# Kernel optimization log

Measured on AMD Instinct MI355X. Metric: run time of the kernel, lower is better.

The kernel has to match this reference:

```python
import jax, jax.numpy as jnp
import numpy as np

NUM_ENT = 50000
NUM_REL = 200          # init_rel has 2*NUM_REL rows (fwd + inverse)
D = 200                # init_dim = gcn_dim = embed_dim
B = 1024
E_HALF = 250000        # edges per direction; total 2*E_HALF
PERM = 1
K_H, K_W = 20, 10      # 2*k_w*k_h == 2*embed_dim
NUM_FILT = 96
KER = 9
FLAT_SZ = K_H * 2 * K_W * NUM_FILT * PERM  # 38400


def _bn(x, g, b, axes):
    # batch-norm with batch statistics (training-mode math, no running stats)
    m = jnp.mean(x, axes, keepdims=True)
    v = jnp.var(x, axes, keepdims=True)
    return (x - m) * jax.lax.rsqrt(v + 1e-5) * g + b


def setup_inputs() -> dict:
    key = jax.random.key(0)
    ks = jax.random.split(key, 24)
    rng = np.random.default_rng(0)
    # graph (constants)
    s = jax.random.randint(ks[0], (E_HALF,), 0, NUM_ENT)
    d = jax.random.randint(ks[1], (E_HALF,), 0, NUM_ENT)
    t = jax.random.randint(ks[2], (E_HALF,), 0, NUM_REL)
    edge_index = jnp.stack([jnp.concatenate([s, d]), jnp.concatenate([d, s])])  # [2, 2*E_HALF]
    edge_type = jnp.concatenate([t, t + NUM_REL])
    chequer_perm = jnp.asarray(np.stack([rng.permutation(2 * D) for _ in range(PERM)]), dtype=jnp.int32)
    # batch indices
    sub = jax.random.randint(ks[3], (B,), 0, NUM_ENT)
    rel = jax.random.randint(ks[4], (B,), 0, 2 * NUM_REL)
    neg_ents = jax.random.randint(ks[5], (B,), 0, NUM_ENT)
    n = lambda k, shp, sc=0.05: jax.random.normal(ks[k], shp, jnp.float32) * sc
    return {
        'sub': sub, 'rel': rel, 'neg_ents': neg_ents,
        'edge_index': edge_index, 'edge_type': edge_type, 'chequer_perm': chequer_perm,
        'init_embed': n(6, (NUM_ENT, D)),
        'init_rel': n(7, (2 * NUM_REL, D)),
        'w_in': n(8, (D, D)), 'w_out': n(9, (D, D)), 'w_loop': n(10, (D, D)),
        'w_rel': n(11, (D, D)), 'loop_rel': n(12, (1, D)),
        'bn0_g': jnp.ones((PERM,)), 'bn0_b': jnp.zeros((PERM,)),
        'bn1_g': jnp.ones((NUM_FILT * PERM,)), 'bn1_b': jnp.zeros((NUM_FILT * PERM,)),
        'bn2_g': jnp.ones((D,)), 'bn2_b': jnp.zeros((D,)),
        'conv_filt': n(13, (NUM_FILT, 1, KER, KER), 0.1),
        'fc_w': n(14, (D, FLAT_SZ), 0.01), 'fc_b': jnp.zeros((D,)),
        'bias_ent': jnp.zeros((NUM_ENT,)),
    }


def _forward(init_embed, init_rel, w_in, w_out, w_loop, w_rel, loop_rel,
             bn0_g, bn0_b, bn1_g, bn1_b, bn2_g, bn2_b,
             conv_filt, fc_w, fc_b, bias_ent,
             sub, rel, edge_index, edge_type, chequer_perm):
    # ---- GPKGConv encoder (CompGCN-style, op='sub', eval mode -> dropout off) ----
    src, dst = edge_index[0], edge_index[1]
    msg = init_embed[src] - init_rel[edge_type]                      # [E, D] irregular gather
    msg = jnp.concatenate([msg[:E_HALF] @ w_in, msg[E_HALF:] @ w_out], axis=0)
    deg = jax.ops.segment_sum(jnp.ones(msg.shape[0], msg.dtype), dst, num_segments=NUM_ENT)
    dinv = jnp.where(deg > 0, jax.lax.rsqrt(jnp.maximum(deg, 1.0)), 0.0)
    norm = (dinv[src] * dinv[dst])[:, None]
    agg = jax.ops.segment_sum(msg * norm, dst, num_segments=NUM_ENT)  # irregular scatter
    loop_msg = (init_embed - loop_rel) @ w_loop
    all_ent = jnp.tanh((agg + loop_msg) / 3.0)                        # [num_ent, D]
    r = init_rel @ w_rel                                              # [2*num_rel, D]
    # ---- InteractE-style chequer conv decoder ----
    sub_emb = all_ent[sub]
    rel_emb = r[rel]
    comb = jnp.concatenate([sub_emb, rel_emb], axis=1)                # [B, 2D]
    cheq = jnp.take(comb, chequer_perm, axis=1)                       # [B, perm, 2D]
    x = cheq.reshape(-1, PERM, 2 * K_W, K_H)
    x = _bn(x, bn0_g.reshape(1, -1, 1, 1), bn0_b.reshape(1, -1, 1, 1), (0, 2, 3))
    pad = KER // 2
    x = jnp.pad(x, ((0, 0), (0, 0), (pad, pad), (pad, pad)), mode='wrap')  # circular pad
    filt = jnp.tile(conv_filt, (PERM, 1, 1, 1))
    x = jax.lax.conv_general_dilated(x, filt, (1, 1), 'VALID',
                                     dimension_numbers=('NCHW', 'OIHW', 'NCHW'),
                                     feature_group_count=PERM)        # [B, 96, 20, 20]
    x = _bn(x, bn1_g.reshape(1, -1, 1, 1), bn1_b.reshape(1, -1, 1, 1), (0, 2, 3))
    x = jax.nn.relu(x)
    x = x.reshape(x.shape[0], -1) @ fc_w.T + fc_b                     # [B, D]
    x = _bn(x, bn2_g, bn2_b, (0,))
    x = jax.nn.relu(x)
    logits = x @ all_ent.T + bias_ent                                 # [B, num_ent]
    return jax.nn.sigmoid(logits)


def reference(sub, rel, neg_ents, edge_index, edge_type, chequer_perm,
              init_embed, init_rel, w_in, w_out, w_loop, w_rel, loop_rel,
              bn0_g, bn0_b, bn1_g, bn1_b, bn2_g, bn2_b,
              conv_filt, fc_w, fc_b, bias_ent):
    return _forward(init_embed, init_rel, w_in, w_out, w_loop, w_rel, loop_rel,
                    bn0_g, bn0_b, bn1_g, bn1_b, bn2_g, bn2_b,
                    conv_filt, fc_w, fc_b, bias_ent,
                    sub, rel, edge_index, edge_type, chequer_perm)
```

## Files before the change

### kernel.cpp

```cpp
#include <hip/hip_runtime.h>

#define ETOT  500000
#define EHALF 250000
#define NENT  50000
#define NSEG  (2 * NENT)
#define DD    200
#define BB    1024
#define NF    96
#define FLAT  38400

#define FC_KS     20
#define FC_KSLICE 1920
#define FC_NCHUNK 60

#define LE 64

#define OFF_AGG      0LL
#define ZSTART       20000000LL
#define OFF_CNT      20000000LL
#define OFF_ACC0     20100004LL
#define OFF_ACC1     20100006LL
#define ZEND         20100198LL
#define OFF_CURSOR   20304998LL
#define OFF_BSUM     20404998LL
#define OFF_ELIST    20405126LL
#define OFF_WT       20405128LL
#define OFF_DINV     20905126LL
#define OFF_RMAT     20955126LL
#define OFF_CHEQ     21035126LL
#define OFF_BN1S     21444726LL
#define OFF_X2H      21649720LL
#define OFF_X2L      21752120LL

#define OD_CONV 0LL
#define OD_FWH  39321600LL
#define OD_FWL  43161600LL
#define OD_PART 47001600LL

typedef __attribute__((ext_vector_type(8))) short bf16x8;
typedef __attribute__((ext_vector_type(4))) float f32x4;

__device__ inline void bf16split(float v, ushort& h, ushort& l) {
    unsigned u = __float_as_uint(v);
    unsigned hu = u & 0xffff0000u;
    h = (ushort)(hu >> 16);
    float lf = v - __uint_as_float(hu);
    l = (ushort)(__float_as_uint(lf) >> 16);
}

__device__ inline void split8(const float* e, bf16x8& h8, bf16x8& l8) {
#pragma unroll
    for (int t = 0; t < 8; t++) {
        ushort h, l;
        bf16split(e[t], h, l);
        h8[t] = (short)h;
        l8[t] = (short)l;
    }
}


__global__ void k_hist(const int* __restrict__ ei, int* __restrict__ cnt) {
    int e = blockIdx.x * 256 + threadIdx.x;
    if (e < ETOT) {
        int seg = (e < EHALF ? 0 : NENT) + ei[ETOT + e];
        atomicAdd(&cnt[seg], 1);
    }
}

__global__ void k_dinv(const int* __restrict__ cnt, float* __restrict__ dinv) {
    int i = blockIdx.x * 256 + threadIdx.x;
    if (i < NENT) {
        int d = cnt[i] + cnt[NENT + i];
        dinv[i] = d > 0 ? rsqrtf((float)d) : 0.f;
    }
}

__global__ void k_scan1(int* __restrict__ cnt, int* __restrict__ bsum) {
    __shared__ int S[256];
    int base = blockIdx.x * 1024 + threadIdx.x * 4;
    int v[4], s = 0;
#pragma unroll
    for (int i = 0; i < 4; i++) { v[i] = (base + i <= NSEG) ? cnt[base + i] : 0; s += v[i]; }
    S[threadIdx.x] = s;
    __syncthreads();
    for (int off = 1; off < 256; off <<= 1) {
        int t = (threadIdx.x >= off) ? S[threadIdx.x - off] : 0;
        __syncthreads();
        S[threadIdx.x] += t;
        __syncthreads();
    }
    int run = S[threadIdx.x] - s;
#pragma unroll
    for (int i = 0; i < 4; i++) {
        if (base + i <= NSEG) cnt[base + i] = run;
        run += v[i];
    }
    if (threadIdx.x == 255) bsum[blockIdx.x] = S[255];
}

__global__ void k_scan2(int* __restrict__ bsum) {
    __shared__ int S[128];
    int v = (threadIdx.x < 98) ? bsum[threadIdx.x] : 0;
    S[threadIdx.x] = v;
    __syncthreads();
    for (int off = 1; off < 128; off <<= 1) {
        int t = (threadIdx.x >= off) ? S[threadIdx.x - off] : 0;
        __syncthreads();
        S[threadIdx.x] += t;
        __syncthreads();
    }
    if (threadIdx.x < 98) bsum[threadIdx.x] = S[threadIdx.x] - v;
}

__global__ void k_scan3(int* __restrict__ cnt, const int* __restrict__ bsum,
                        int* __restrict__ cursor) {
    int add = bsum[blockIdx.x];
    int base = blockIdx.x * 1024 + threadIdx.x * 4;
#pragma unroll
    for (int i = 0; i < 4; i++) {
        int idx = base + i;
        if (idx <= NSEG) {
            int v = cnt[idx] + add;
            cnt[idx] = v;
            if (idx < NSEG) cursor[idx] = v;
        }
    }
}

__global__ void k_fill(const int* __restrict__ ei, int* __restrict__ cursor,
                       int* __restrict__ elist) {
    int e = blockIdx.x * 256 + threadIdx.x;
    if (e < ETOT) {
        int seg = (e < EHALF ? 0 : NENT) + ei[ETOT + e];
        int pos = atomicAdd(&cursor[seg], 1);
        elist[pos] = e;
    }
}

__global__ void k_agg(const int* __restrict__ ei, const int* __restrict__ et,
                      const int* __restrict__ row_start, const int* __restrict__ elist,
                      const float* __restrict__ emb, const float* __restrict__ rel,
                      const float* __restrict__ dinv, float* __restrict__ agg) {
    int seg = blockIdx.x * 4 + (threadIdx.x >> 6);
    int lane = threadIdx.x & 63;
    int dst = seg - (seg >= NENT ? NENT : 0);
    float dd = dinv[dst];
    int s = row_start[seg], e = row_start[seg + 1];
    bool act = lane < 50;
    float4 acc = {0.f, 0.f, 0.f, 0.f};
    for (int i = s; i < e; i++) {
        int ed = elist[i];
        int src = ei[ed];
        int t = et[ed];
        float nrm = dinv[src] * dd;
        if (act) {
            float4 a = *(const float4*)&emb[(long long)src * DD + lane * 4];
            float4 b = *(const float4*)&rel[t * DD + lane * 4];
            acc.x += (a.x - b.x) * nrm;
            acc.y += (a.y - b.y) * nrm;
            acc.z += (a.z - b.z) * nrm;
            acc.w += (a.w - b.w) * nrm;
        }
    }
    if (act) *(float4*)&agg[(long long)seg * DD + lane * 4] = acc;
}


__global__ void k_cvt3w(const float* __restrict__ w_in, const float* __restrict__ w_out,
                        const float* __restrict__ w_loop,
                        ushort* __restrict__ wth, ushort* __restrict__ wtl) {
    int idx = blockIdx.x * 256 + threadIdx.x;
    if (idx >= 3 * DD * DD) return;
    int s = idx / (DD * DD);
    int rem = idx - s * DD * DD;
    int j = rem / DD, k = rem - (rem / DD) * DD;
    const float* w = (s == 0) ? w_in : (s == 1) ? w_out : w_loop;
    ushort h, l;
    bf16split(w[k * DD + j], h, l);
    wth[idx] = h;
    wtl[idx] = l;
}

__global__ __launch_bounds__(256) void k_allent_mfma(
        const float* __restrict__ agg, const float* __restrict__ emb,
        const float* __restrict__ loop_rel,
        const ushort* __restrict__ wth, const ushort* __restrict__ wtl,
        float* __restrict__ all_ent) {
    __shared__ __align__(16) ushort Bh[2][112][36];
    __shared__ __align__(16) ushort Bl[2][112][36];
    __shared__ float lr[DD];
    int tid = threadIdx.x;
    for (int i = tid; i < DD; i += 256) lr[i] = loop_rel[i];
    int wid = tid >> 6, lane = tid & 63, l15 = lane & 15, q = lane >> 4;
    int r0 = blockIdx.x * 64;
    int nh = blockIdx.y;
    int row = r0 + wid * 16 + l15;
    if (row > NENT - 1) row = NENT - 1;
    const float* apa = &agg[(long long)row * DD];
    const float* apb = &agg[(long long)(NENT + row) * DD];
    const float* apc = &emb[(long long)row * DD];

    bool stg = tid < 224;
    int srow = tid - (tid >= 112 ? 112 : 0);
    if (srow > 111) srow = 0;
    bool spl = (tid >= 112) && stg;
    int sj = nh * 112 + srow;
    int sjr = sj < DD ? sj : DD - 1;
    const ushort* bplane = spl ? wtl : wth;
    int srowoff = sjr * DD;
    ushort* d0 = spl ? &Bl[0][srow][0] : &Bh[0][srow][0];
    ushort* d1 = spl ? &Bl[1][srow][0] : &Bh[1][srow][0];

    f32x4 zero4 = {0.f, 0.f, 0.f, 0.f};
    f32x4 acc[7];
#pragma unroll
    for (int n = 0; n < 7; n++) acc[n] = zero4;

    uint4 w0 = {0u,0u,0u,0u}, w1 = {0u,0u,0u,0u}, w2 = {0u,0u,0u,0u}, w3 = {0u,0u,0u,0u};
    if (stg) {
        const ushort* src = bplane + srowoff;
        w0 = *(const uint4*)&src[0];
        w1 = *(const uint4*)&src[8];
        w2 = *(const uint4*)&src[16];
        w3 = *(const uint4*)&src[24];
        *(uint4*)&d0[0]  = w0;
        *(uint4*)&d0[8]  = w1;
        *(uint4*)&d0[16] = w2;
        *(uint4*)&d0[24] = w3;
    }
    float4 a1, a2;
    {
        int k0 = q * 8;
        a1 = *(const float4*)&apa[k0];
        a2 = *(const float4*)&apa[k0 + 4];
    }
    __syncthreads();

    for (int t = 0; t < 21; t++) {
        int buf = t & 1;
        int s = t / 7, kk = t - s * 7;
        bool prt = (kk == 6);
        int k0 = prt ? 192 : kk * 32 + q * 8;
        bool act = !prt || (q == 0);
        bool more = (t + 1 < 21);
        if (stg && more) {
            int t2 = t + 1, ss = t2 / 7, k2 = t2 - ss * 7;
            bool p2 = (k2 == 6);
            int koff2 = p2 ? 192 : k2 * 32;
            const ushort* src = bplane + ss * (DD * DD) + srowoff + koff2;
            uint4 zz = {0u,0u,0u,0u};
            w0 = *(const uint4*)&src[0];
            w1 = p2 ? zz : *(const uint4*)&src[8];
            w2 = p2 ? zz : *(const uint4*)&src[16];
            w3 = p2 ? zz : *(const uint4*)&src[24];
        }
        float4 n1 = {0.f, 0.f, 0.f, 0.f}, n2 = {0.f, 0.f, 0.f, 0.f};
        if (more) {
            int t2 = t + 1, ss = t2 / 7, k2 = t2 - ss * 7;
            bool p2 = (k2 == 6);
            int ka = p2 ? 192 : k2 * 32 + q * 8;
            const float* apn = (ss == 0) ? apa : (ss == 1) ? apb : apc;
            if (!p2 || q == 0) {
                n1 = *(const float4*)&apn[ka];
                n2 = *(const float4*)&apn[ka + 4];
            }
        }
        float e[8] = {0.f, 0.f, 0.f, 0.f, 0.f, 0.f, 0.f, 0.f};
        if (act) {
            float4 v1 = a1, v2 = a2;
            if (s == 2) {
                float4 u1 = *(const float4*)&lr[k0];
                float4 u2 = *(const float4*)&lr[k0 + 4];
                v1.x -= u1.x; v1.y -= u1.y; v1.z -= u1.z; v1.w -= u1.w;
                v2.x -= u2.x; v2.y -= u2.y; v2.z -= u2.z; v2.w -= u2.w;
            }
            e[0] = v1.x; e[1] = v1.y; e[2] = v1.z; e[3] = v1.w;
            e[4] = v2.x; e[5] = v2.y; e[6] = v2.z; e[7] = v2.w;
        }
        bf16x8 ah, al;
        split8(e, ah, al);
#pragma unroll
        for (int n = 0; n < 7; n++) {
            bf16x8 bh = *(const bf16x8*)&Bh[buf][n * 16 + l15][q * 8];
            bf16x8 bl = *(const bf16x8*)&Bl[buf][n * 16 + l15][q * 8];
            acc[n] = __builtin_amdgcn_mfma_f32_16x16x32_bf16(ah, bh, acc[n], 0, 0, 0);
            acc[n] = __builtin_amdgcn_mfma_f32_16x16x32_bf16(ah, bl, acc[n], 0, 0, 0);
            acc[n] = __builtin_amdgcn_mfma_f32_16x16x32_bf16(al, bh, acc[n], 0, 0, 0);
        }
        if (stg && more) {
            ushort* d = buf ? d0 : d1;
            *(uint4*)&d[0]  = w0;
            *(uint4*)&d[8]  = w1;
            *(uint4*)&d[16] = w2;
            *(uint4*)&d[24] = w3;
        }
        __syncthreads();
        a1 = n1; a2 = n2;
    }
#pragma unroll
    for (int n = 0; n < 7; n++) {
        int j = nh * 112 + n * 16 + l15;
        if (j < DD) {
            int rowb = r0 + wid * 16 + q * 4;
#pragma unroll
            for (int r = 0; r < 4; r++) {
                if (rowb + r < NENT)
                    all_ent[(long long)(rowb + r) * DD + j] = tanhf(acc[n][r] * (1.f / 3.f));
            }
        }
    }
}

__global__ void k_cvt(const float* __restrict__ src, ushort* __restrict__ hi,
                      ushort* __restrict__ lo) {
    long long i = (long long)(blockIdx.x * 256 + threadIdx.x) * 4;
    if (i >= (long long)NENT * DD) return;
    float4 v = *(const float4*)&src[i];
    ushort4 h, l;
    bf16split(v.x, h.x, l.x);
    bf16split(v.y, h.y, l.y);
    bf16split(v.z, h.z, l.z);
    bf16split(v.w, h.w, l.w);
    *(ushort4*)&hi[i] = h;
    *(ushort4*)&lo[i] = l;
}

__global__ void k_cvtw(const float* __restrict__ src, ushort* __restrict__ hi,
                       ushort* __restrict__ lo) {
    long long i = (long long)(blockIdx.x * 256 + threadIdx.x) * 4;
    if (i >= (long long)DD * FLAT) return;
    float4 v = *(const float4*)&src[i];
    ushort4 h, l;
    bf16split(v.x, h.x, l.x);
    bf16split(v.y, h.y, l.y);
    bf16split(v.z, h.z, l.z);
    bf16split(v.w, h.w, l.w);
    *(ushort4*)&hi[i] = h;
    *(ushort4*)&lo[i] = l;
}

__global__ void k_rmat(const float* __restrict__ init_rel, const float* __restrict__ w_rel,
                       float* __restrict__ rmat) {
    __shared__ float S[16][DD];
    int r0 = blockIdx.x * 16;
    for (int i = threadIdx.x; i < 16 * DD; i += 256)
        S[i / DD][i % DD] = init_rel[(r0 + i / DD) * DD + i % DD];
    __syncthreads();
    int j = threadIdx.x;
    if (j < DD) {
        float acc[16];
#pragma unroll
        for (int rr = 0; rr < 16; rr++) acc[rr] = 0.f;
        for (int k = 0; k < DD; k += 4) {
            float wx = w_rel[(k + 0) * DD + j], wy = w_rel[(k + 1) * DD + j],
                  wz = w_rel[(k + 2) * DD + j], ww = w_rel[(k + 3) * DD + j];
#pragma unroll
            for (int rr = 0; rr < 16; rr++) {
                float4 a = *(const float4*)&S[rr][k];
                acc[rr] += a.x * wx + a.y * wy + a.z * wz + a.w * ww;
            }
        }
#pragma unroll
        for (int rr = 0; rr < 16; rr++) rmat[(r0 + rr) * DD + j] = acc[rr];
    }
}


__global__ void k_cheq(const int* __restrict__ sub, const int* __restrict__ rel,
                       const int* __restrict__ perm, const float* __restrict__ all_ent,
                       const float* __restrict__ rmat, float* __restrict__ cheq,
                       float* __restrict__ acc0) {
    int i = blockIdx.x * 256 + threadIdx.x;
    int b = i / 400, p = i % 400;
    int c = perm[p];
    float v = (c < DD) ? all_ent[(long long)sub[b] * DD + c]
                       : rmat[rel[b] * DD + (c - DD)];
    cheq[i] = v;
    __shared__ float s1[256], s2[256];
    s1[threadIdx.x] = v;
    s2[threadIdx.x] = v * v;
    __syncthreads();
    for (int st = 128; st > 0; st >>= 1) {
        if (threadIdx.x < st) { s1[threadIdx.x] += s1[threadIdx.x + st]; s2[threadIdx.x] += s2[threadIdx.x + st]; }
        __syncthreads();
    }
    if (threadIdx.x == 0) { atomicAdd(&acc0[0], s1[0]); atomicAdd(&acc0[1], s2[0]); }
}

__global__ void k_conv(const float* __restrict__ cheq, const float* __restrict__ acc0,
                       const float* __restrict__ bn0_g, const float* __restrict__ bn0_b,
                       const float* __restrict__ filt, float* __restrict__ conv_out,
                       float* __restrict__ acc1) {
    __shared__ __align__(16) float xp[28][36];
    __shared__ float fl[NF * 81];
    __shared__ float csum[NF], csq[NF];
    int b = blockIdx.x;
    const float invN = 1.f / (BB * 400.f);
    float mean = acc0[0] * invN;
    float var = acc0[1] * invN - mean * mean;
    float sc = rsqrtf(var + 1e-5f) * bn0_g[0];
    float sh = bn0_b[0] - mean * sc;
    for (int i = threadIdx.x; i < 28 * 28; i += 256) {
        int r = i / 28, c = i % 28;
        int rr = (r + 16) % 20, cc = (c + 16) % 20;
        xp[r][c] = cheq[b * 400 + rr * 20 + cc] * sc + sh;
    }
    for (int i = threadIdx.x; i < NF * 81; i += 256) fl[i] = filt[i];
    if (threadIdx.x < NF) { csum[threadIdx.x] = 0.f; csq[threadIdx.x] = 0.f; }
    __syncthreads();
    for (int t = threadIdx.x; t < NF * 20; t += 256) {
        int ch = t / 20, row = t % 20;
        float acc[20];
#pragma unroll
        for (int c2 = 0; c2 < 20; c2++) acc[c2] = 0.f;
        for (int di = 0; di < 9; di++) {
            float xr[28];
#pragma unroll
            for (int g = 0; g < 7; g++) {
                float4 v = *(const float4*)&xp[row + di][g * 4];
                xr[g * 4 + 0] = v.x; xr[g * 4 + 1] = v.y;
                xr[g * 4 + 2] = v.z; xr[g * 4 + 3] = v.w;
            }
            float f[9];
#pragma unroll
            for (int dj = 0; dj < 9; dj++) f[dj] = fl[ch * 81 + di * 9 + dj];
#pragma unroll
            for (int dj = 0; dj < 9; dj++)
#pragma unroll
                for (int c2 = 0; c2 < 20; c2++)
                    acc[c2] = fmaf(xr[c2 + dj], f[dj], acc[c2]);
        }
        float s = 0.f, q = 0.f;
        long long base = (long long)b * FLAT + ch * 400 + row * 20;
#pragma unroll
        for (int c2 = 0; c2 < 20; c2++) {
            float v = acc[c2];
            s += v; q += v * v;
            conv_out[base + c2] = v;
        }
        atomicAdd(&csum[ch], s);
        atomicAdd(&csq[ch], q);
    }
    __syncthreads();
    if (threadIdx.x < NF) {
        atomicAdd(&acc1[threadIdx.x], csum[threadIdx.x]);
        atomicAdd(&acc1[NF + threadIdx.x], csq[threadIdx.x]);
    }
}

__global__ void k_bn1fin(const float* __restrict__ acc1, const float* __restrict__ g1,
                         const float* __restrict__ b1, float* __restrict__ bn1s) {
    int c = threadIdx.x;
    if (c >= NF) return;
    const float invN = 1.f / (BB * 400.f);
    float m = acc1[c] * invN;
    float v = acc1[NF + c] * invN - m * m;
    float sc = rsqrtf(v + 1e-5f) * g1[c];
    bn1s[c] = sc;
    bn1s[NF + c] = b1[c] - m * sc;
}

__global__ __launch_bounds__(256) void k_fc_mfma(
        const float* __restrict__ conv_out, const float* __restrict__ bn1s,
        const ushort* __restrict__ fwh, const ushort* __restrict__ fwl,
        float* __restrict__ part) {
    __shared__ __align__(16) ushort Bh[2][112][36];
    __shared__ __align__(16) ushort Bl[2][112][36];
    __shared__ float bns[192];
    int tid = threadIdx.x;
    for (int i = tid; i < 192; i += 256) bns[i] = bn1s[i];
    int wid = tid >> 6, lane = tid & 63, l15 = lane & 15, q = lane >> 4;
    int b0 = blockIdx.x * 64;
    int nh = blockIdx.y;
    int ksl = blockIdx.z;
    int kbase = ksl * FC_KSLICE;

    const float* ap = conv_out + (long long)(b0 + wid * 16 + l15) * FLAT;

    bool stg = tid < 224;
    int srow = tid - (tid >= 112 ? 112 : 0);
    if (srow > 111) srow = 0;
    bool spl = (tid >= 112) && stg;
    int sj = nh * 112 + srow;
    int sjr = sj < DD ? sj : DD - 1;
    const ushort* bsrc = (spl ? fwl : fwh) + (long long)sjr * FLAT + kbase;
    ushort* d0 = spl ? &Bl[0][srow][0] : &Bh[0][srow][0];
    ushort* d1 = spl ? &Bl[1][srow][0] : &Bh[1][srow][0];

    f32x4 zero4 = {0.f, 0.f, 0.f, 0.f};
    f32x4 acc[7];
#pragma unroll
    for (int n = 0; n < 7; n++) acc[n] = zero4;

    uint4 s0 = {0u,0u,0u,0u}, s1 = {0u,0u,0u,0u}, s2 = {0u,0u,0u,0u}, s3 = {0u,0u,0u,0u};
    if (stg) {
        s0 = *(const uint4*)&bsrc[0];
        s1 = *(const uint4*)&bsrc[8];
        s2 = *(const uint4*)&bsrc[16];
        s3 = *(const uint4*)&bsrc[24];
        *(uint4*)&d0[0]  = s0;
        *(uint4*)&d0[8]  = s1;
        *(uint4*)&d0[16] = s2;
        *(uint4*)&d0[24] = s3;
    }
    float4 a1, a2;
    {
        int k0 = kbase + q * 8;
        a1 = *(const float4*)&ap[k0];
        a2 = *(const float4*)&ap[k0 + 4];
    }
    __syncthreads();

    for (int c = 0; c < FC_NCHUNK; c++) {
        int buf = c & 1;
        int kc = kbase + c * 32 + q * 8;
        bool more = (c + 1 < FC_NCHUNK);
        if (stg && more) {
            int kn = (c + 1) * 32;
            s0 = *(const uint4*)&bsrc[kn];
            s1 = *(const uint4*)&bsrc[kn + 8];
            s2 = *(const uint4*)&bsrc[kn + 16];
            s3 = *(const uint4*)&bsrc[kn + 24];
        }
        float4 n1 = {0.f, 0.f, 0.f, 0.f}, n2 = {0.f, 0.f, 0.f, 0.f};
        if (more) {
            n1 = *(const float4*)&ap[kc + 32];
            n2 = *(const float4*)&ap[kc + 36];
        }
        int ch = kc / 400;
        float sc = bns[ch], sh = bns[96 + ch];
        float e[8] = {
            fmaxf(a1.x * sc + sh, 0.f), fmaxf(a1.y * sc + sh, 0.f),
            fmaxf(a1.z * sc + sh, 0.f), fmaxf(a1.w * sc + sh, 0.f),
            fmaxf(a2.x * sc + sh, 0.f), fmaxf(a2.y * sc + sh, 0.f),
            fmaxf(a2.z * sc + sh, 0.f), fmaxf(a2.w * sc + sh, 0.f)};
        bf16x8 ah, al;
        split8(e, ah, al);
#pragma unroll
        for (int n = 0; n < 7; n++) {
            bf16x8 bh = *(const bf16x8*)&Bh[buf][n * 16 + l15][q * 8];
            bf16x8 bl = *(const bf16x8*)&Bl[buf][n * 16 + l15][q * 8];
            acc[n] = __builtin_amdgcn_mfma_f32_16x16x32_bf16(ah, bh, acc[n], 0, 0, 0);
            acc[n] = __builtin_amdgcn_mfma_f32_16x16x32_bf16(ah, bl, acc[n], 0, 0, 0);
            acc[n] = __builtin_amdgcn_mfma_f32_16x16x32_bf16(al, bh, acc[n], 0, 0, 0);
        }
        if (stg && more) {
            ushort* d = buf ? d0 : d1;
            *(uint4*)&d[0]  = s0;
            *(uint4*)&d[8]  = s1;
            *(uint4*)&d[16] = s2;
            *(uint4*)&d[24] = s3;
        }
        __syncthreads();
        a1 = n1; a2 = n2;
    }
    long long pbase = (long long)ksl * (BB * DD);
#pragma unroll
    for (int n = 0; n < 7; n++) {
        int j = nh * 112 + n * 16 + l15;
        if (j < DD) {
            int rowb = b0 + wid * 16 + q * 4;
#pragma unroll
            for (int r = 0; r < 4; r++)
                part[pbase + (long long)(rowb + r) * DD + j] = acc[n][r];
        }
    }
}

__global__ void k_bn2(const float* __restrict__ part, const float* __restrict__ fc_b,
                      const float* __restrict__ g2, const float* __restrict__ b2,
                      ushort* __restrict__ x2h, ushort* __restrict__ x2l) {
    int j = blockIdx.x;
    float vals[4];
    float s = 0.f, q = 0.f;
#pragma unroll
    for (int i = 0; i < 4; i++) {
        int b = threadIdx.x + i * 256;
        float v = fc_b[j];
#pragma unroll
        for (int ks = 0; ks < FC_KS; ks++)
            v += part[(long long)ks * (BB * DD) + (long long)b * DD + j];
        vals[i] = v;
        s += v; q += v * v;
    }
    __shared__ float r1[256], r2[256];
    __shared__ float bc[2];
    r1[threadIdx.x] = s; r2[threadIdx.x] = q;
    __syncthreads();
    for (int st = 128; st > 0; st >>= 1) {
        if (threadIdx.x < st) { r1[threadIdx.x] += r1[threadIdx.x + st]; r2[threadIdx.x] += r2[threadIdx.x + st]; }
        __syncthreads();
    }
    if (threadIdx.x == 0) {
        float m = r1[0] * (1.f / BB);
        float v = r2[0] * (1.f / BB) - m * m;
        float sc = rsqrtf(v + 1e-5f) * g2[j];
        bc[0] = sc; bc[1] = b2[j] - m * sc;
    }
    __syncthreads();
    float sc = bc[0], sh = bc[1];
#pragma unroll
    for (int i = 0; i < 4; i++) {
        int b = threadIdx.x + i * 256;
        float v = fmaxf(vals[i] * sc + sh, 0.f);
        ushort h, l;
        bf16split(v, h, l);
        x2h[b * DD + j] = h;
        x2l[b * DD + j] = l;
    }
}

__global__ __launch_bounds__(512) void k_logits_mfma(
        const ushort* __restrict__ x2h, const ushort* __restrict__ x2l,
        const ushort* __restrict__ aeh, const ushort* __restrict__ ael,
        const float* __restrict__ bias, float* __restrict__ out) {
    __shared__ ushort Bhs[LE * DD];
    __shared__ ushort Bls[LE * DD];
    __shared__ __align__(16) float Tw[8][16][36];
    int e0 = blockIdx.x * LE;
    for (int i = threadIdx.x; i < 2 * LE * 25; i += 512) {
        int pl = i >= LE * 25;
        int ii = pl ? i - LE * 25 : i;
        int row = ii / 25, seg = ii % 25;
        int e = e0 + row;
        if (e > NENT - 1) e = NENT - 1;
        const ushort* src = (pl ? ael : aeh) + (long long)e * DD + seg * 8;
        uint4 v = *(const uint4*)src;
        if (pl) *(uint4*)&Bls[row * DD + seg * 8] = v;
        else    *(uint4*)&Bhs[row * DD + seg * 8] = v;
    }
    __syncthreads();

    int wid = threadIdx.x >> 6;
    int lane = threadIdx.x & 63;
    int l15 = lane & 15, q = lane >> 4;
    int wm = wid >> 1;
    int wn = wid & 1;

    int nbase0 = (wn * 32 + l15) * DD;
    int nbase1 = (wn * 32 + 16 + l15) * DD;

    int tr = lane >> 3;
    int tc = (lane & 7) * 4;
    int ceg = e0 + wn * 32 + tc;
    bool cval = ceg < NENT;
    float4 bb = {0.f, 0.f, 0.f, 0.f};
    if (cval) bb = *(const float4*)&bias[ceg];

    f32x4 zero4 = {0.f, 0.f, 0.f, 0.f};
    bf16x8 zf = {0, 0, 0, 0, 0, 0, 0, 0};
    const int STEP = 128 * DD;

    const ushort* ah0 = x2h + (long long)(wm * 32 + l15) * DD;
    const ushort* al0 = x2l + (long long)(wm * 32 + l15) * DD;
    const ushort* ah1 = ah0 + 16 * DD;
    const ushort* al1 = al0 + 16 * DD;

    bf16x8 pa_h0, pa_l0, pa_h1, pa_l1;
    {
        int k0 = q * 8;
        pa_h0 = *(const bf16x8*)&ah0[k0];
        pa_l0 = *(const bf16x8*)&al0[k0];
        pa_h1 = *(const bf16x8*)&ah1[k0];
        pa_l1 = *(const bf16x8*)&al1[k0];
    }

    for (int it = 0; it < 8; it++) {
        f32x4 acc00 = zero4, acc01 = zero4, acc10 = zero4, acc11 = zero4;
#pragma unroll
        for (int kk = 0; kk < 6; kk++) {
            int kn = (kk < 5) ? (kk + 1) * 32 + q * 8 : 192;
            bf16x8 na_h0 = *(const bf16x8*)&ah0[kn];
            bf16x8 na_l0 = *(const bf16x8*)&al0[kn];
            bf16x8 na_h1 = *(const bf16x8*)&ah1[kn];
            bf16x8 na_l1 = *(const bf16x8*)&al1[kn];
            int kb = kk * 32 + q * 8;
            bf16x8 bh0 = *(const bf16x8*)&Bhs[nbase0 + kb];
            bf16x8 bl0 = *(const bf16x8*)&Bls[nbase0 + kb];
            bf16x8 bh1 = *(const bf16x8*)&Bhs[nbase1 + kb];
            bf16x8 bl1 = *(const bf16x8*)&Bls[nbase1 + kb];
            acc00 = __builtin_amdgcn_mfma_f32_16x16x32_bf16(pa_h0, bh0, acc00, 0, 0, 0);
            acc00 = __builtin_amdgcn_mfma_f32_16x16x32_bf16(pa_h0, bl0, acc00, 0, 0, 0);
            acc00 = __builtin_amdgcn_mfma_f32_16x16x32_bf16(pa_l0, bh0, acc00, 0, 0, 0);
            acc01 = __builtin_amdgcn_mfma_f32_16x16x32_bf16(pa_h0, bh1, acc01, 0, 0, 0);
            acc01 = __builtin_amdgcn_mfma_f32_16x16x32_bf16(pa_h0, bl1, acc01, 0, 0, 0);
            acc01 = __builtin_amdgcn_mfma_f32_16x16x32_bf16(pa_l0, bh1, acc01, 0, 0, 0);
            acc10 = __builtin_amdgcn_mfma_f32_16x16x32_bf16(pa_h1, bh0, acc10, 0, 0, 0);
            acc10 = __builtin_amdgcn_mfma_f32_16x16x32_bf16(pa_h1, bl0, acc10, 0, 0, 0);
            acc10 = __builtin_amdgcn_mfma_f32_16x16x32_bf16(pa_l1, bh0, acc10, 0, 0, 0);
            acc11 = __builtin_amdgcn_mfma_f32_16x16x32_bf16(pa_h1, bh1, acc11, 0, 0, 0);
            acc11 = __builtin_amdgcn_mfma_f32_16x16x32_bf16(pa_h1, bl1, acc11, 0, 0, 0);
            acc11 = __builtin_amdgcn_mfma_f32_16x16x32_bf16(pa_l1, bh1, acc11, 0, 0, 0);
            pa_h0 = na_h0; pa_l0 = na_l0; pa_h1 = na_h1; pa_l1 = na_l1;
        }
        {
            bf16x8 na_h0 = zf, na_l0 = zf, na_h1 = zf, na_l1 = zf;
            if (it + 1 < 8) {
                int k0 = q * 8;
                na_h0 = *(const bf16x8*)&ah0[STEP + k0];
                na_l0 = *(const bf16x8*)&al0[STEP + k0];
                na_h1 = *(const bf16x8*)&ah1[STEP + k0];
                na_l1 = *(const bf16x8*)&al1[STEP + k0];
            }
            bool a0 = (q == 0);
            bf16x8 xh0 = a0 ? pa_h0 : zf, xl0 = a0 ? pa_l0 : zf;
            bf16x8 xh1 = a0 ? pa_h1 : zf, xl1 = a0 ? pa_l1 : zf;
            bf16x8 bh0 = a0 ? *(const bf16x8*)&Bhs[nbase0 + 192] : zf;
            bf16x8 bl0 = a0 ? *(const bf16x8*)&Bls[nbase0 + 192] : zf;
            bf16x8 bh1 = a0 ? *(const bf16x8*)&Bhs[nbase1 + 192] : zf;
            bf16x8 bl1 = a0 ? *(const bf16x8*)&Bls[nbase1 + 192] : zf;
            acc00 = __builtin_amdgcn_mfma_f32_16x16x32_bf16(xh0, bh0, acc00, 0, 0, 0);
            acc00 = __builtin_amdgcn_mfma_f32_16x16x32_bf16(xh0, bl0, acc00, 0, 0, 0);
            acc00 = __builtin_amdgcn_mfma_f32_16x16x32_bf16(xl0, bh0, acc00, 0, 0, 0);
            acc01 = __builtin_amdgcn_mfma_f32_16x16x32_bf16(xh0, bh1, acc01, 0, 0, 0);
            acc01 = __builtin_amdgcn_mfma_f32_16x16x32_bf16(xh0, bl1, acc01, 0, 0, 0);
            acc01 = __builtin_amdgcn_mfma_f32_16x16x32_bf16(xl0, bh1, acc01, 0, 0, 0);
            acc10 = __builtin_amdgcn_mfma_f32_16x16x32_bf16(xh1, bh0, acc10, 0, 0, 0);
            acc10 = __builtin_amdgcn_mfma_f32_16x16x32_bf16(xh1, bl0, acc10, 0, 0, 0);
            acc10 = __builtin_amdgcn_mfma_f32_16x16x32_bf16(xl1, bh0, acc10, 0, 0, 0);
            acc11 = __builtin_amdgcn_mfma_f32_16x16x32_bf16(xh1, bh1, acc11, 0, 0, 0);
            acc11 = __builtin_amdgcn_mfma_f32_16x16x32_bf16(xh1, bl1, acc11, 0, 0, 0);
            acc11 = __builtin_amdgcn_mfma_f32_16x16x32_bf16(xl1, bh1, acc11, 0, 0, 0);
            pa_h0 = na_h0; pa_l0 = na_l0; pa_h1 = na_h1; pa_l1 = na_l1;
        }
        {
#pragma unroll
            for (int r = 0; r < 4; r++) {
                Tw[wid][q * 4 + r][l15] = acc00[r];
                Tw[wid][q * 4 + r][16 + l15] = acc01[r];
            }
            float4 v0 = *(const float4*)&Tw[wid][tr][tc];
            float4 v1 = *(const float4*)&Tw[wid][8 + tr][tc];
            if (cval) {
                int rg0 = it * 128 + wm * 32 + tr;
                float4 o0, o1;
                o0.x = 1.f / (1.f + __expf(-(v0.x + bb.x)));
                o0.y = 1.f / (1.f + __expf(-(v0.y + bb.y)));
                o0.z = 1.f / (1.f + __expf(-(v0.z + bb.z)));
                o0.w = 1.f / (1.f + __expf(-(v0.w + bb.w)));
                o1.x = 1.f / (1.f + __expf(-(v1.x + bb.x)));
                o1.y = 1.f / (1.f + __expf(-(v1.y + bb.y)));
                o1.z = 1.f / (1.f + __expf(-(v1.z + bb.z)));
                o1.w = 1.f / (1.f + __expf(-(v1.w + bb.w)));
                *(float4*)&out[(long long)rg0 * NENT + ceg] = o0;
                *(float4*)&out[(long long)(rg0 + 8) * NENT + ceg] = o1;
            }
        }
        {
#pragma unroll
            for (int r = 0; r < 4; r++) {
                Tw[wid][q * 4 + r][l15] = acc10[r];
                Tw[wid][q * 4 + r][16 + l15] = acc11[r];
            }
            float4 v0 = *(const float4*)&Tw[wid][tr][tc];
            float4 v1 = *(const float4*)&Tw[wid][8 + tr][tc];
            if (cval) {
                int rg0 = it * 128 + wm * 32 + 16 + tr;
                float4 o0, o1;
                o0.x = 1.f / (1.f + __expf(-(v0.x + bb.x)));
                o0.y = 1.f / (1.f + __expf(-(v0.y + bb.y)));
                o0.z = 1.f / (1.f + __expf(-(v0.z + bb.z)));
                o0.w = 1.f / (1.f + __expf(-(v0.w + bb.w)));
                o1.x = 1.f / (1.f + __expf(-(v1.x + bb.x)));
                o1.y = 1.f / (1.f + __expf(-(v1.y + bb.y)));
                o1.z = 1.f / (1.f + __expf(-(v1.z + bb.z)));
                o1.w = 1.f / (1.f + __expf(-(v1.w + bb.w)));
                *(float4*)&out[(long long)rg0 * NENT + ceg] = o0;
                *(float4*)&out[(long long)(rg0 + 8) * NENT + ceg] = o1;
            }
        }
        ah0 += STEP; al0 += STEP; ah1 += STEP; al1 += STEP;
    }
}


extern "C" void kernel_launch(void* const* d_in, const int* in_sizes, int n_in,
                              void* d_out, int out_size, void* d_ws, size_t ws_size,
                              hipStream_t stream) {
    const int*   sub      = (const int*)d_in[0];
    const int*   rel      = (const int*)d_in[1];
    const int*   ei       = (const int*)d_in[3];
    const int*   et       = (const int*)d_in[4];
    const int*   perm     = (const int*)d_in[5];
    const float* emb      = (const float*)d_in[6];
    const float* init_rel = (const float*)d_in[7];
    const float* w_in     = (const float*)d_in[8];
    const float* w_out    = (const float*)d_in[9];
    const float* w_loop   = (const float*)d_in[10];
    const float* w_rel    = (const float*)d_in[11];
    const float* loop_rel = (const float*)d_in[12];
    const float* bn0_g    = (const float*)d_in[13];
    const float* bn0_b    = (const float*)d_in[14];
    const float* bn1_g    = (const float*)d_in[15];
    const float* bn1_b    = (const float*)d_in[16];
    const float* bn2_g    = (const float*)d_in[17];
    const float* bn2_b    = (const float*)d_in[18];
    const float* filt     = (const float*)d_in[19];
    const float* fc_w     = (const float*)d_in[20];
    const float* fc_b     = (const float*)d_in[21];
    const float* bias_ent = (const float*)d_in[22];

    float* ws  = (float*)d_ws;
    float* o   = (float*)d_out;

    float* agg     = ws + OFF_AGG;
    float* agg_out = agg + (long long)NENT * DD;
    int*   cnt     = (int*)(ws + OFF_CNT);
    int*   cursor  = (int*)(ws + OFF_CURSOR);
    int*   bsum    = (int*)(ws + OFF_BSUM);
    int*   elist   = (int*)(ws + OFF_ELIST);
    ushort* wth    = (ushort*)(ws + OFF_WT);
    ushort* wtl    = wth + 3 * DD * DD;
    float* acc0    = ws + OFF_ACC0;
    float* acc1    = ws + OFF_ACC1;
    float* dinv    = ws + OFF_DINV;
    float* rmat    = ws + OFF_RMAT;
    float* cheq    = ws + OFF_CHEQ;
    float* bn1s    = ws + OFF_BN1S;
    ushort* x2h    = (ushort*)(ws + OFF_X2H);
    ushort* x2l    = (ushort*)(ws + OFF_X2L);
    ushort* aeh    = (ushort*)agg_out;
    ushort* ael    = aeh + (long long)NENT * DD;

    float*  all_ent  = o + OD_CONV;
    float*  conv_out = o + OD_CONV;
    ushort* fwh      = (ushort*)(o + OD_FWH);
    ushort* fwl      = (ushort*)(o + OD_FWL);
    float*  part     = o + OD_PART;

    hipMemsetAsync(ws + ZSTART, 0, (size_t)(ZEND - ZSTART) * 4, stream);

    k_hist<<<(ETOT + 255) / 256, 256, 0, stream>>>(ei, cnt);
    k_dinv<<<(NENT + 255) / 256, 256, 0, stream>>>(cnt, dinv);
    k_scan1<<<98, 256, 0, stream>>>(cnt, bsum);
    k_scan2<<<1, 128, 0, stream>>>(bsum);
    k_scan3<<<98, 256, 0, stream>>>(cnt, bsum, cursor);
    k_fill<<<(ETOT + 255) / 256, 256, 0, stream>>>(ei, cursor, elist);
    k_agg<<<NSEG / 4, 256, 0, stream>>>(ei, et, cnt, elist, emb, init_rel, dinv, agg);

    k_cvt3w<<<(3 * DD * DD + 255) / 256, 256, 0, stream>>>(w_in, w_out, w_loop, wth, wtl);
    k_allent_mfma<<<dim3((NENT + 63) / 64, 2), 256, 0, stream>>>(agg, emb, loop_rel,
                                                                 wth, wtl, all_ent);
    k_cvt<<<((NENT * DD / 4) + 255) / 256, 256, 0, stream>>>(all_ent, aeh, ael);
    k_cvtw<<<((DD * FLAT / 4) + 255) / 256, 256, 0, stream>>>(fc_w, fwh, fwl);
    k_rmat<<<400 / 16, 256, 0, stream>>>(init_rel, w_rel, rmat);

    k_cheq<<<(BB * 400) / 256, 256, 0, stream>>>(sub, rel, perm, all_ent, rmat, cheq, acc0);
    k_conv<<<BB, 256, 0, stream>>>(cheq, acc0, bn0_g, bn0_b, filt, conv_out, acc1);
    k_bn1fin<<<1, 128, 0, stream>>>(acc1, bn1_g, bn1_b, bn1s);
    k_fc_mfma<<<dim3(BB / 64, 2, FC_KS), 256, 0, stream>>>(conv_out, bn1s, fwh, fwl, part);
    k_bn2<<<DD, 256, 0, stream>>>(part, fc_b, bn2_g, bn2_b, x2h, x2l);
    k_logits_mfma<<<(NENT + LE - 1) / LE, 512, 0, stream>>>(
        x2h, x2l, aeh, ael, bias_ent, o);
}
```

Measured before the change: 847.6 us.

## Merge FC N-halves into one 512-thread block and prefetch edge indices in aggregation

```diff
diff --git a/kernel.cpp b/kernel.cpp
--- a/kernel.cpp
+++ b/kernel.cpp
@@ -148,18 +148,26 @@
     int s = row_start[seg], e = row_start[seg + 1];
     bool act = lane < 50;
     float4 acc = {0.f, 0.f, 0.f, 0.f};
-    for (int i = s; i < e; i++) {
-        int ed = elist[i];
+    if (s < e) {
+        int ed = elist[s];
         int src = ei[ed];
         int t = et[ed];
-        float nrm = dinv[src] * dd;
-        if (act) {
-            float4 a = *(const float4*)&emb[(long long)src * DD + lane * 4];
-            float4 b = *(const float4*)&rel[t * DD + lane * 4];
-            acc.x += (a.x - b.x) * nrm;
-            acc.y += (a.y - b.y) * nrm;
-            acc.z += (a.z - b.z) * nrm;
-            acc.w += (a.w - b.w) * nrm;
+        for (int i = s; i < e; i++) {
+            int src_c = src, t_c = t;
+            if (i + 1 < e) {
+                int ed2 = elist[i + 1];
+                src = ei[ed2];
+                t = et[ed2];
+            }
+            float nrm = dinv[src_c] * dd;
+            if (act) {
+                float4 a = *(const float4*)&emb[(long long)src_c * DD + lane * 4];
+                float4 b = *(const float4*)&rel[t_c * DD + lane * 4];
+                acc.x += (a.x - b.x) * nrm;
+                acc.y += (a.y - b.y) * nrm;
+                acc.z += (a.z - b.z) * nrm;
+                acc.w += (a.w - b.w) * nrm;
+            }
         }
     }
     if (act) *(float4*)&agg[(long long)seg * DD + lane * 4] = acc;
@@ -460,29 +468,29 @@
     bn1s[NF + c] = b1[c] - m * sc;
 }
 
-__global__ __launch_bounds__(256) void k_fc_mfma(
+__global__ __launch_bounds__(512) void k_fc_mfma(
         const float* __restrict__ conv_out, const float* __restrict__ bn1s,
         const ushort* __restrict__ fwh, const ushort* __restrict__ fwl,
         float* __restrict__ part) {
-    __shared__ __align__(16) ushort Bh[2][112][36];
-    __shared__ __align__(16) ushort Bl[2][112][36];
+    __shared__ __align__(16) ushort Bh[2][224][36];
+    __shared__ __align__(16) ushort Bl[2][224][36];
     __shared__ float bns[192];
     int tid = threadIdx.x;
-    for (int i = tid; i < 192; i += 256) bns[i] = bn1s[i];
+    for (int i = tid; i < 192; i += 512) bns[i] = bn1s[i];
     int wid = tid >> 6, lane = tid & 63, l15 = lane & 15, q = lane >> 4;
+    int wm = wid >> 1;
+    int wnh = wid & 1;
     int b0 = blockIdx.x * 64;
-    int nh = blockIdx.y;
-    int ksl = blockIdx.z;
+    int ksl = blockIdx.y;
     int kbase = ksl * FC_KSLICE;
 
-    const float* ap = conv_out + (long long)(b0 + wid * 16 + l15) * FLAT;
-
-    bool stg = tid < 224;
-    int srow = tid - (tid >= 112 ? 112 : 0);
-    if (srow > 111) srow = 0;
-    bool spl = (tid >= 112) && stg;
-    int sj = nh * 112 + srow;
-    int sjr = sj < DD ? sj : DD - 1;
+    const float* ap = conv_out + (long long)(b0 + wm * 16 + l15) * FLAT;
+
+    bool stg = tid < 448;
+    bool spl = (tid >= 224) && stg;
+    int srow = spl ? tid - 224 : tid;
+    if (srow > 223) srow = 0;
+    int sjr = srow < DD ? srow : DD - 1;
     const ushort* bsrc = (spl ? fwl : fwh) + (long long)sjr * FLAT + kbase;
     ushort* d0 = spl ? &Bl[0][srow][0] : &Bh[0][srow][0];
     ushort* d1 = spl ? &Bl[1][srow][0] : &Bh[1][srow][0];
@@ -538,8 +546,9 @@
         split8(e, ah, al);
 #pragma unroll
         for (int n = 0; n < 7; n++) {
-            bf16x8 bh = *(const bf16x8*)&Bh[buf][n * 16 + l15][q * 8];
-            bf16x8 bl = *(const bf16x8*)&Bl[buf][n * 16 + l15][q * 8];
+            int brow = wnh * 112 + n * 16 + l15;
+            bf16x8 bh = *(const bf16x8*)&Bh[buf][brow][q * 8];
+            bf16x8 bl = *(const bf16x8*)&Bl[buf][brow][q * 8];
             acc[n] = __builtin_amdgcn_mfma_f32_16x16x32_bf16(ah, bh, acc[n], 0, 0, 0);
             acc[n] = __builtin_amdgcn_mfma_f32_16x16x32_bf16(ah, bl, acc[n], 0, 0, 0);
             acc[n] = __builtin_amdgcn_mfma_f32_16x16x32_bf16(al, bh, acc[n], 0, 0, 0);
@@ -557,9 +566,9 @@
     long long pbase = (long long)ksl * (BB * DD);
 #pragma unroll
     for (int n = 0; n < 7; n++) {
-        int j = nh * 112 + n * 16 + l15;
+        int j = wnh * 112 + n * 16 + l15;
         if (j < DD) {
-            int rowb = b0 + wid * 16 + q * 4;
+            int rowb = b0 + wm * 16 + q * 4;
 #pragma unroll
             for (int r = 0; r < 4; r++)
                 part[pbase + (long long)(rowb + r) * DD + j] = acc[n][r];
@@ -848,7 +857,7 @@
     k_cheq<<<(BB * 400) / 256, 256, 0, stream>>>(sub, rel, perm, all_ent, rmat, cheq, acc0);
     k_conv<<<BB, 256, 0, stream>>>(cheq, acc0, bn0_g, bn0_b, filt, conv_out, acc1);
     k_bn1fin<<<1, 128, 0, stream>>>(acc1, bn1_g, bn1_b, bn1s);
-    k_fc_mfma<<<dim3(BB / 64, 2, FC_KS), 256, 0, stream>>>(conv_out, bn1s, fwh, fwl, part);
+    k_fc_mfma<<<dim3(BB / 64, FC_KS), 512, 0, stream>>>(conv_out, bn1s, fwh, fwl, part);
     k_bn2<<<DD, 256, 0, stream>>>(part, fc_b, bn2_g, bn2_b, x2h, x2l);
     k_logits_mfma<<<(NENT + LE - 1) / LE, 512, 0, stream>>>(
         x2h, x2l, aeh, ael, bias_ent, o);
```

Result: no change. 859.9 us (+1.5%).
